# Kernel tuning notes

Measured on AMD Instinct MI355X. Metric: run time of the kernel, lower is better.

Reference implementation:

```python
import jax, jax.numpy as jnp
import numpy as np

D_RBF = 36
KMIN = 9
EPS_LN = 1e-5


def layer_norm(x, g, b):
    mu = x.mean(-1, keepdims=True)
    var = ((x - mu) ** 2).mean(-1, keepdims=True)
    return (x - mu) * jax.lax.rsqrt(var + EPS_LN) * g + b


def rbf(D):
    # radial basis expansion, 36 gaussians on [0, 20]
    mu = jnp.linspace(0.0, 20.0, D_RBF)
    sigma = 20.0 / D_RBF
    return jnp.exp(-(((D[..., None] - mu) / sigma) ** 2))


def cdist(a, b):
    d2 = jnp.sum((a[:, :, None, :] - b[:, None, :, :]) ** 2, -1)
    return jnp.sqrt(jnp.maximum(d2, 1e-12))


def setup_inputs() -> dict:
    key = jax.random.key(0)
    ks = iter(jax.random.split(key, 64))
    B, N, L = 1, 64, 512
    d_msa, d_pair, d_state = 64, 128, 16
    def nrm(shape, s=1.0):
        return jax.random.normal(next(ks), shape, jnp.float32) * s
    def lin(fin, fout):
        return nrm((fin, fout), 0.05), jnp.zeros((fout,), jnp.float32)
    def ln(d):
        return jnp.ones((d,), jnp.float32), jnp.zeros((d,), jnp.float32)
    inp = {}
    inp['msa'] = nrm((B, N, L, d_msa))
    inp['pair'] = nrm((B, L, L, d_pair))
    inp['xyz'] = nrm((B, L, 3, 3), 8.0)  # spread coords so kNN is meaningful
    inp['state'] = nrm((B, L, d_state))
    inp['seq1hot'] = jax.nn.one_hot(jax.random.randint(next(ks), (B, L), 0, 21), 21, dtype=jnp.float32)
    inp['idx'] = jnp.broadcast_to(jnp.arange(L, dtype=jnp.int32)[None], (B, L))
    inp['top_k'] = 64
    inp['g_msa'], inp['b_msa'] = ln(d_msa)
    inp['g_pair'], inp['b_pair'] = ln(d_pair)
    inp['g_state'], inp['b_state'] = ln(d_state)
    inp['Wq'], inp['bq'] = lin(d_msa, d_msa)
    inp['Wk'], inp['bk'] = lin(d_msa, d_msa)
    inp['Wx'], inp['bx'] = lin(d_msa + 21 + d_state, 32)
    inp['We1'], inp['be1'] = lin(d_pair, 32)
    inp['We2'], inp['be2'] = lin(32 + D_RBF + 1, 32)
    inp['g_node'], inp['b_node'] = ln(32)
    inp['g_e1'], inp['b_e1'] = ln(32)
    inp['g_e2'], inp['b_e2'] = ln(32)
    # SE3-style equivariant MP layer params
    inp['Wm1'], inp['bm1'] = lin(32 + 32 + 32 + 1, 64)
    inp['Wm2'], inp['bm2'] = lin(64, 32)
    inp['Wc'], inp['bc'] = lin(32, 8)      # 2 out vec channels x (1 coef for d + 3 for v_src)
    inp['Wh'], inp['bh'] = lin(64, 16)     # l0 out
    inp['Wv'] = nrm((2, 3), 0.05)          # l1 channel mixing
    return inp


def reference(msa, pair, xyz, state, seq1hot, idx, top_k,
              g_msa, b_msa, g_pair, b_pair, g_state, b_state,
              Wq, bq, Wk, bk, Wx, bx, We1, be1, We2, be2,
              g_node, b_node, g_e1, b_e1, g_e2, b_e2,
              Wm1, bm1, Wm2, bm2, Wc, bc, Wh, bh, Wv):
    eps = 1e-5
    B, N, L, K = msa.shape
    msa = layer_norm(msa, g_msa, b_msa)
    pair = layer_norm(pair, g_pair, b_pair)
    state = layer_norm(state, g_state, b_state)

    # SequenceWeight (1 head): first-seq query attends over N sequences per position
    q = (msa[:, 0] @ Wq + bq) / jnp.sqrt(jnp.float32(K))       # (B,L,K)
    k = jnp.einsum('bnlk,kd->bnld', msa, Wk) + bk              # (B,N,L,K)
    attn = jax.nn.softmax(jnp.einsum('blk,bnlk->bnl', q, k), axis=1)
    msa1 = jnp.einsum('bnl,bnlk->blk', attn, msa)              # (B,L,K)

    node = jnp.concatenate([msa1, seq1hot, state], -1)
    node = layer_norm(node @ Wx + bx, g_node, b_node)          # (B,L,32)
    edge = layer_norm(pair @ We1 + be1, g_e1, b_e1)            # (B,L,L,32)

    sep = idx[:, None, :] - idx[:, :, None]                    # (B,L,L)
    neighbor = jnp.where(jnp.abs(sep) <= 1, sep, 0).astype(node.dtype)[..., None]
    ca = xyz[:, :, 1]                                          # (B,L,3)
    rbf_feat = rbf(cdist(ca, ca))
    edge = jnp.concatenate([edge, rbf_feat, neighbor], -1)
    edge = layer_norm(edge @ We2 + be2, g_e2, b_e2)            # (B,L,L,32)

    # kNN + sequence-separation graph, as a dense boolean mask (edge i->j)
    eye = jnp.eye(L)[None]
    D = cdist(ca, ca) + eye * 999.9
    sep_a = jnp.abs(sep).astype(jnp.float32) + eye * 999.9
    kk = min(int(top_k), L)
    _, E_idx = jax.lax.top_k(-jax.lax.stop_gradient(D), kk)    # (B,L,kk) nearest j per i
    bi = jnp.arange(B)[:, None, None]
    ii = jnp.arange(L)[None, :, None]
    mask = jnp.zeros((B, L, L), bool).at[bi, ii, E_idx].set(True)
    mask = jnp.logical_or(mask, sep_a < KMIN)
    maskf = mask.astype(node.dtype)

    v = xyz - ca[:, :, None, :]                                # l1 feats (B,L,3,3)
    dvec = jax.lax.stop_gradient(ca[:, None, :, :] - ca[:, :, None, :])  # d[b,i,j]=ca_j-ca_i
    dist = jnp.linalg.norm(dvec, axis=-1, keepdims=True)       # (B,L,L,1)

    # invariant scalar messages (avoid materializing concat: split Wm1)
    hid = (node @ Wm1[:32])[:, :, None, :] + (node @ Wm1[32:64])[:, None, :, :] \
        + edge @ Wm1[64:96] + dist * Wm1[96] + bm1
    hid = jax.nn.relu(hid)                                     # (B,L,L,64)
    m = jax.nn.relu(hid @ Wm2 + bm2)                           # (B,L,L,32)
    coef = (m @ Wc + bc).reshape(B, L, L, 2, 4)
    # equivariant vector messages: coef0 * d_ij + sum_c coef_c * v_i[c]
    vmsg = coef[..., 0:1] * dvec[:, :, :, None, :] \
         + jnp.einsum('bijoc,bicv->bijov', coef[..., 1:], v)   # (B,L,L,2,3)
    agg_m = jnp.einsum('bij,bijk->bjk', maskf, m)              # aggregate at target j
    agg_v = jnp.einsum('bij,bijov->bjov', maskf, vmsg)

    state_out = jnp.concatenate([node, agg_m], -1) @ Wh + bh   # shift['0'] -> (B,L,16)
    off = agg_v + jnp.einsum('oc,blcv->blov', Wv, v)           # shift['1'] -> (B,L,2,3)

    # Rodrigues rotation + translation update
    T = off[:, :, 0]
    R = off[:, :, 1]
    ang = jnp.linalg.norm(R, axis=-1, keepdims=True)           # (B,L,1)
    Rv = (R / (ang + eps))[:, :, None, :]                      # (B,L,1,3)
    Rdv = jnp.sum(Rv * v, -1, keepdims=True)                   # (B,L,3,1)
    Rxv = jnp.cross(jnp.broadcast_to(Rv, v.shape), v)
    vperp = v - Rv * Rdv
    upar = Rv * Rdv
    c = jnp.cos(ang)[:, :, None, :]
    s = jnp.sin(ang)[:, :, None, :]
    v_new = vperp * c + Rxv * s + upar
    xyz_new = v_new + (ca + T)[:, :, None, :]
    return xyz_new, state_out
```

## Files before the change

### kernel.cpp

```cpp
#include <hip/hip_runtime.h>
#include <hip/hip_bf16.h>

typedef __attribute__((ext_vector_type(8))) short short8v;
typedef __attribute__((ext_vector_type(4))) float f32x4;

__device__ __forceinline__ unsigned short f2bu(float a){
  union { __hip_bfloat16 b; unsigned short u; } cv;
  cv.b = __float2bfloat16(a);
  return cv.u;
}
__device__ __forceinline__ void sp2(float a, unsigned short &h, unsigned short &l){
  h = f2bu(a);
  l = f2bu(a - __uint_as_float(((unsigned)h)<<16));
}
__device__ __forceinline__ float wred64(float v){
  #pragma unroll
  for(int o=32;o;o>>=1) v += __shfl_xor(v,o,64);
  return v;
}
__device__ __forceinline__ float wred32(float v){
  #pragma unroll
  for(int o=16;o;o>>=1) v += __shfl_xor(v,o,64);
  return v;
}
__device__ __forceinline__ float wmax64(float v){
  #pragma unroll
  for(int o=32;o;o>>=1) v = fmaxf(v,__shfl_xor(v,o,64));
  return v;
}

__global__ void __launch_bounds__(256) k_ctx(
  const float* __restrict__ msa, const float* __restrict__ g_msa, const float* __restrict__ b_msa,
  const float* __restrict__ Wq, const float* __restrict__ bq,
  const float* __restrict__ Wk, const float* __restrict__ bk,
  const float* __restrict__ seq1hot, const float* __restrict__ state,
  const float* __restrict__ g_state, const float* __restrict__ b_state,
  const float* __restrict__ Wx, const float* __restrict__ bx,
  const float* __restrict__ g_node, const float* __restrict__ b_node,
  const float* __restrict__ Wm1, const float* __restrict__ xyz,
  float* __restrict__ node, float* __restrict__ nodeA, float* __restrict__ nodeB,
  float* __restrict__ ca, float* __restrict__ vv)
{
  int l = blockIdx.x, tid = threadIdx.x;
  int wave = tid>>6, lane = tid&63;
  __shared__ float ms[64][64];
  __shared__ float qs[64];
  __shared__ float logit[64];
  __shared__ float part[4][64];
  __shared__ float ins[101];
  __shared__ float nd[32];

  {
    int nn = tid>>2, qd = tid&3;
    const float* mrow = msa + ((size_t)nn*512 + (size_t)l)*64 + qd*16;
    f32x4 a[4];
    #pragma unroll
    for(int t=0;t<4;t++) a[t] = *(const f32x4*)(mrow + t*4);
    float s=0.f, ss=0.f;
    #pragma unroll
    for(int t=0;t<4;t++)
      #pragma unroll
      for(int e=0;e<4;e++){ float v=a[t][e]; s+=v; ss+=v*v; }
    s  += __shfl_xor(s,1,64);  s  += __shfl_xor(s,2,64);
    ss += __shfl_xor(ss,1,64); ss += __shfl_xor(ss,2,64);
    float mu = s*(1.f/64.f);
    float rstd = rsqrtf(ss*(1.f/64.f) - mu*mu + 1e-5f);
    #pragma unroll
    for(int t=0;t<4;t++){
      f32x4 g4 = *(const f32x4*)(g_msa + qd*16 + t*4);
      f32x4 b4 = *(const f32x4*)(b_msa + qd*16 + t*4);
      f32x4 o4;
      #pragma unroll
      for(int e=0;e<4;e++) o4[e] = (a[t][e]-mu)*rstd*g4[e] + b4[e];
      *(f32x4*)&ms[nn][qd*16 + t*4] = o4;
    }
  }
  __syncthreads();
  if(wave==0){
    float acc = bq[lane];
    for(int k=0;k<64;k++) acc += ms[0][k]*Wq[k*64+lane];
    qs[lane] = acc*0.125f;
  }
  __syncthreads();
  float qd2 = qs[lane];
  for(int it=0; it<16; ++it){
    int nn = it*4 + wave;
    float acc = bk[lane];
    for(int k2=0;k2<64;k2++) acc += ms[nn][k2]*Wk[k2*64+lane];
    float p = wred64(qd2*acc);
    if(lane==0) logit[nn] = p;
  }
  __syncthreads();
  float v  = logit[lane];
  float mx = wmax64(v);
  float e  = expf(v-mx);
  float sd = wred64(e);
  float a  = e/sd;
  float pm = 0.f;
  for(int it=0; it<16; ++it){
    int nn = it*4 + wave;
    pm += __shfl(a,nn,64)*ms[nn][lane];
  }
  part[wave][lane] = pm;
  __syncthreads();
  if(wave==0){
    ins[lane] = part[0][lane]+part[1][lane]+part[2][lane]+part[3][lane];
    if(lane<21) ins[64+lane] = seq1hot[l*21+lane];
    float sv = (lane<16)? state[l*16+lane] : 0.f;
    float mu = sv;
    #pragma unroll
    for(int o=8;o;o>>=1) mu += __shfl_xor(mu,o,64);
    mu *= (1.f/16.f);
    float dv = sv-mu;
    float var = dv*dv;
    #pragma unroll
    for(int o=8;o;o>>=1) var += __shfl_xor(var,o,64);
    var *= (1.f/16.f);
    if(lane<16) ins[85+lane] = dv*rsqrtf(var+1e-5f)*g_state[lane]+b_state[lane];

    int d = lane & 31;
    float np_ = 0.f;
    if(lane<32){
      np_ = bx[d];
      for(int c=0;c<101;c++) np_ += ins[c]*Wx[c*32+d];
    }
    float mu2 = wred32(np_)*(1.f/32.f);
    float d2  = np_-mu2;
    float v2  = wred32(d2*d2)*(1.f/32.f);
    float nv  = d2*rsqrtf(v2+1e-5f);
    if(lane<32){
      nv = nv*g_node[d]+b_node[d];
      node[l*32+d] = nv;
      nd[d] = nv;
    }
    float a2=0.f, b2=0.f;
    for(int c=0;c<32;c++){
      float x = nd[c];
      a2 += x*Wm1[c*64+lane];
      b2 += x*Wm1[(32+c)*64+lane];
    }
    nodeA[l*64+lane] = a2;
    nodeB[l*64+lane] = b2;
    if(lane<3) ca[l*3+lane] = xyz[l*9+3+lane];
    if(lane<9) vv[l*9+lane] = xyz[l*9+lane] - xyz[l*9+3+(lane%3)];
  }
}

__global__ void k_topk(const float* __restrict__ ca, const int* __restrict__ idx,
                       const int* __restrict__ topk_ptr, unsigned char* __restrict__ maskT){
  int i = blockIdx.x, lane = threadIdx.x;
  float cx = ca[i*3], cy = ca[i*3+1], cz = ca[i*3+2];
  int idxi = idx[i];
  unsigned long long key[8];
  #pragma unroll
  for(int t=0;t<8;t++){
    int jj = t*64 + lane;
    float dx = cx-ca[jj*3], dy = cy-ca[jj*3+1], dz = cz-ca[jj*3+2];
    float dd = sqrtf(fmaxf(dx*dx+dy*dy+dz*dz, 1e-12f));
    if(jj==i) dd += 999.9f;
    key[t] = (((unsigned long long)__float_as_uint(dd))<<32) | (unsigned)jj;
    int sep = abs(idx[jj]-idxi);
    maskT[jj*512+i] = (jj!=i && sep<9) ? 1 : 0;
  }
  int kk = *topk_ptr; if(kk>512) kk = 512;
  for(int t=0;t<kk;t++){
    unsigned long long m = key[0];
    #pragma unroll
    for(int u=1;u<8;u++) m = (key[u]<m)? key[u] : m;
    #pragma unroll
    for(int o=32;o;o>>=1){
      unsigned long long o2 = __shfl_xor(m,o,64);
      m = (o2<m)? o2 : m;
    }
    int jc = (int)(m & 0xffffffffu);
    if(lane==0) maskT[jc*512+i] = 1;
    #pragma unroll
    for(int u=0;u<8;u++) if(key[u]==m) key[u] = ~0ull;
  }
}

__global__ void k_fold(const float* __restrict__ We1, const float* __restrict__ be1,
                       const float* __restrict__ g_pair, const float* __restrict__ b_pair,
                       const float* __restrict__ We2, const float* __restrict__ be2,
                       const float* __restrict__ g_e1, const float* __restrict__ b_e1,
                       const float* __restrict__ Wm1, const float* __restrict__ bm1,
                       const float* __restrict__ g_e2, const float* __restrict__ b_e2,
                       const float* __restrict__ Wm2, const float* __restrict__ Wc,
                       unsigned short* __restrict__ wbuf, float* __restrict__ bbuf){
  int fidx = blockIdx.x;
  int tid  = threadIdx.x;
  if(fidx < 46){
    int t = fidx*512 + tid;
    int lane = tid>>3, e = tid&7;
    int f = (fidx<23)? fidx : fidx-23;
    int krow = (lane>>4)*8 + e;
    int n = lane&15;
    float val = 0.f;
    if(f<8){
      int kt=f>>1, nt=f&1; int c=kt*32+krow, d=nt*16+n;
      val = g_pair[c]*We1[c*32+d];
    } else if(f<14){
      int f2=f-8; int kt=f2>>1, nt=f2&1; int c=kt*32+krow, d=nt*16+n;
      if(c<32)      val = g_e1[c]*We2[c*32+d];
      else if(c<69) val = We2[c*32+d];
      else          val = 0.f;
    } else if(f<18){
      int nt=f-14; int c=krow, h=nt*16+n;
      val = g_e2[c]*Wm1[(64+c)*64+h];
    } else if(f<22){
      int f2=f-18; int kt=f2>>1, nt=f2&1; int c=kt*32+krow, d=nt*16+n;
      val = Wm2[c*32+d];
    } else {
      int c=krow;
      val = (n<8)? Wc[c*8+n] : 0.f;
    }
    unsigned short h = f2bu(val);
    if(fidx<23) wbuf[t] = h;
    else {
      float fh = __uint_as_float(((unsigned)h)<<16);
      wbuf[t] = f2bu(val - fh);
    }
  } else {
    if(tid<32){
      float s = be1[tid];
      for(int c=0;c<128;c++) s += b_pair[c]*We1[c*32+tid];
      bbuf[tid]=s;
    } else if(tid<64){
      int d=tid-32; float s=be2[d];
      for(int c=0;c<32;c++) s += b_e1[c]*We2[c*32+d];
      bbuf[tid]=s;
    } else if(tid<128){
      int h=tid-64; float s=bm1[h];
      for(int c=0;c<32;c++) s += b_e2[c]*Wm1[(64+c)*64+h];
      bbuf[tid]=s;
    }
  }
}

__global__ void __launch_bounds__(256,2) k_pair_mfma(
  const float* __restrict__ pair, const unsigned short* __restrict__ wbuf,
  const float* __restrict__ bbuf, const float* __restrict__ Wm1,
  const float* __restrict__ bm2, const float* __restrict__ bc,
  const float* __restrict__ nodeA, const float* __restrict__ nodeB,
  const float* __restrict__ ca, const float* __restrict__ vv,
  const int* __restrict__ idx, const unsigned char* __restrict__ maskT,
  float* __restrict__ aggM, float* __restrict__ aggV)
{
  const int j = blockIdx.x, tid = threadIdx.x;
  const int wave = tid>>6, lane = tid&63;
  const int kg = lane>>4, n = lane&15;

  __shared__ __align__(16) unsigned short Yh[4][16*104];
  __shared__ __align__(16) unsigned short Yl[4][16*104];
  __shared__ __align__(16) unsigned short WloE[23*512];
  __shared__ float coefT[4][16*8];
  __shared__ float redM[4][32];
  __shared__ float redV[4][8];
  unsigned short* Yhw = Yh[wave];
  unsigned short* Ylw = Yl[wave];
  float* CT = coefT[wave];

  for(int t=tid; t<(23*512)/8; t+=256)
    ((uint4*)WloE)[t] = ((const uint4*)(wbuf + 23*512))[t];

  short8v wf[23];
  #pragma unroll
  for(int f=0; f<23; f++) wf[f] = *(const short8v*)(wbuf + f*512 + lane*8);

  const float be1f0 = bbuf[n],     be1f1 = bbuf[16+n];
  const float be2f0 = bbuf[32+n],  be2f1 = bbuf[48+n];
  float bm1f[4], wm1d[4], nodeBj[4];
  #pragma unroll
  for(int nt=0;nt<4;nt++){
    bm1f[nt]   = bbuf[64+nt*16+n];
    wm1d[nt]   = Wm1[96*64+nt*16+n];
    nodeBj[nt] = nodeB[j*64+nt*16+n];
  }
  const float bm2r0 = bm2[n], bm2r1 = bm2[16+n];
  const float bcr = (n<8)? bc[n] : 0.f;
  const float cjx = ca[j*3], cjy = ca[j*3+1], cjz = ca[j*3+2];
  const int idxj = idx[j];

  __syncthreads();

  for(int t=lane; t<16*27; t+=64){ int r=t/27, c=69+t-r*27; Yhw[r*104+c]=0; Ylw[r*104+c]=0; }

  float accM0=0.f, accM1=0.f;
  float accV[6]={0.f,0.f,0.f,0.f,0.f,0.f};

  float x[4][8];
  {
    const float* prow0 = pair + (((size_t)(wave*16+n))*512 + (size_t)j)*128;
    #pragma unroll
    for(int kt=0;kt<4;kt++){
      *(f32x4*)&x[kt][0] = *(const f32x4*)(prow0 + kt*32 + kg*8);
      *(f32x4*)&x[kt][4] = *(const f32x4*)(prow0 + kt*32 + kg*8 + 4);
    }
  }

  for(int i0 = wave*16; i0 < 512; i0 += 64){
    float s=0.f, ss=0.f;
    #pragma unroll
    for(int kt=0;kt<4;kt++)
      #pragma unroll
      for(int e=0;e<8;e++){ float xv=x[kt][e]; s+=xv; ss+=xv*xv; }
    s  += __shfl_xor(s,16,64);  s  += __shfl_xor(s,32,64);
    ss += __shfl_xor(ss,16,64); ss += __shfl_xor(ss,32,64);
    float mu = s*(1.f/128.f);
    float rstd = rsqrtf(ss*(1.f/128.f) - mu*mu + 1e-5f);
    short8v xh[4], xl[4];
    #pragma unroll
    for(int kt=0;kt<4;kt++){
      #pragma unroll
      for(int e=0;e<8;e++){
        unsigned short h_, l_;
        sp2((x[kt][e]-mu)*rstd, h_, l_);
        xh[kt][e] = (short)h_;
        xl[kt][e] = (short)l_;
      }
    }

    float xn[4][8];
    const bool hasNext = (i0+64 < 512);
    if(hasNext){
      const float* prown = pair + (((size_t)(i0+64+n))*512 + (size_t)j)*128;
      #pragma unroll
      for(int kt=0;kt<4;kt++){
        *(f32x4*)&xn[kt][0] = *(const f32x4*)(prown + kt*32 + kg*8);
        *(f32x4*)&xn[kt][4] = *(const f32x4*)(prown + kt*32 + kg*8 + 4);
      }
    }

    f32x4 z0={0.f,0.f,0.f,0.f}, z1={0.f,0.f,0.f,0.f};
    #pragma unroll
    for(int kt=0;kt<4;kt++){
      short8v wlo0 = *(const short8v*)&WloE[(2*kt+0)*512 + lane*8];
      short8v wlo1 = *(const short8v*)&WloE[(2*kt+1)*512 + lane*8];
      z0 = __builtin_amdgcn_mfma_f32_16x16x32_bf16(xh[kt], wf[2*kt+0], z0, 0,0,0);
      z0 = __builtin_amdgcn_mfma_f32_16x16x32_bf16(xl[kt], wf[2*kt+0], z0, 0,0,0);
      z0 = __builtin_amdgcn_mfma_f32_16x16x32_bf16(xh[kt], wlo0,      z0, 0,0,0);
      z1 = __builtin_amdgcn_mfma_f32_16x16x32_bf16(xh[kt], wf[2*kt+1], z1, 0,0,0);
      z1 = __builtin_amdgcn_mfma_f32_16x16x32_bf16(xl[kt], wf[2*kt+1], z1, 0,0,0);
      z1 = __builtin_amdgcn_mfma_f32_16x16x32_bf16(xh[kt], wlo1,      z1, 0,0,0);
    }
    #pragma unroll
    for(int q=0;q<4;q++){
      float ev0 = z0[q] + be1f0;
      float ev1 = z1[q] + be1f1;
      float sq  = ev0+ev1;
      float sq2 = ev0*ev0+ev1*ev1;
      #pragma unroll
      for(int o=8;o;o>>=1){ sq+=__shfl_xor(sq,o,64); sq2+=__shfl_xor(sq2,o,64); }
      float m_ = sq*(1.f/32.f);
      float rs = rsqrtf(sq2*(1.f/32.f)-m_*m_+1e-5f);
      unsigned short h0,l0,h1,l1;
      sp2((ev0-m_)*rs, h0, l0);
      sp2((ev1-m_)*rs, h1, l1);
      int r = 4*kg+q;
      Yhw[r*104 + n]    = h0;
      Yhw[r*104 + 16+n] = h1;
      Ylw[r*104 + n]    = l0;
      Ylw[r*104 + 16+n] = l1;
    }

    const float* cai = ca + (i0+n)*3;
    float dxr = cjx-cai[0], dyr = cjy-cai[1], dzr = cjz-cai[2];
    float d2r = dxr*dxr+dyr*dyr+dzr*dzr;
    float dist_r = sqrtf(d2r);
    float drbf = sqrtf(fmaxf(d2r,1e-12f));
    #pragma unroll
    for(int sI=0;sI<9;sI++){
      int t = kg*9+sI;
      float u = (drbf - (float)t*(20.f/35.f))*1.8f;
      unsigned short h_, l_;
      sp2(__expf(-u*u), h_, l_);
      Yhw[n*104 + 32 + t] = h_;
      Ylw[n*104 + 32 + t] = l_;
    }
    if(kg==0){
      int sep = idxj - idx[i0+n];
      float nb = (sep>=-1 && sep<=1)?(float)sep:0.f;
      unsigned short h_, l_;
      sp2(nb, h_, l_);
      Yhw[n*104 + 68] = h_;
      Ylw[n*104 + 68] = l_;
    }

    short8v yh_[3], yl_[3];
    #pragma unroll
    for(int kt=0;kt<3;kt++){
      yh_[kt] = *(const short8v*)&Yhw[n*104 + kt*32 + kg*8];
      yl_[kt] = *(const short8v*)&Ylw[n*104 + kt*32 + kg*8];
    }
    f32x4 e2a0={0.f,0.f,0.f,0.f}, e2a1={0.f,0.f,0.f,0.f};
    #pragma unroll
    for(int kt=0;kt<3;kt++){
      short8v wlo0 = *(const short8v*)&WloE[(8+2*kt)*512 + lane*8];
      short8v wlo1 = *(const short8v*)&WloE[(9+2*kt)*512 + lane*8];
      e2a0 = __builtin_amdgcn_mfma_f32_16x16x32_bf16(yh_[kt], wf[8+2*kt], e2a0, 0,0,0);
      e2a0 = __builtin_amdgcn_mfma_f32_16x16x32_bf16(yl_[kt], wf[8+2*kt], e2a0, 0,0,0);
      e2a0 = __builtin_amdgcn_mfma_f32_16x16x32_bf16(yh_[kt], wlo0,      e2a0, 0,0,0);
      e2a1 = __builtin_amdgcn_mfma_f32_16x16x32_bf16(yh_[kt], wf[9+2*kt], e2a1, 0,0,0);
      e2a1 = __builtin_amdgcn_mfma_f32_16x16x32_bf16(yl_[kt], wf[9+2*kt], e2a1, 0,0,0);
      e2a1 = __builtin_amdgcn_mfma_f32_16x16x32_bf16(yh_[kt], wlo1,      e2a1, 0,0,0);
    }
    #pragma unroll
    for(int q=0;q<4;q++){
      float ev0 = e2a0[q]+be2f0;
      float ev1 = e2a1[q]+be2f1;
      float sq  = ev0+ev1;
      float sq2 = ev0*ev0+ev1*ev1;
      #pragma unroll
      for(int o=8;o;o>>=1){ sq+=__shfl_xor(sq,o,64); sq2+=__shfl_xor(sq2,o,64); }
      float m_ = sq*(1.f/32.f);
      float rs = rsqrtf(sq2*(1.f/32.f)-m_*m_+1e-5f);
      unsigned short h0,l0,h1,l1;
      sp2((ev0-m_)*rs, h0, l0);
      sp2((ev1-m_)*rs, h1, l1);
      int r = 4*kg+q;
      Yhw[r*104 + n]    = h0;
      Yhw[r*104 + 16+n] = h1;
      Ylw[r*104 + n]    = l0;
      Ylw[r*104 + 16+n] = l1;
    }

    short8v e2Ah = *(const short8v*)&Yhw[n*104 + kg*8];
    short8v e2Al = *(const short8v*)&Ylw[n*104 + kg*8];
    float dist_q[4];
    #pragma unroll
    for(int q=0;q<4;q++) dist_q[q] = __shfl(dist_r, 4*kg+q, 64);
    #pragma unroll
    for(int nt=0;nt<4;nt++){
      short8v wlo = *(const short8v*)&WloE[(14+nt)*512 + lane*8];
      f32x4 hacc = {0.f,0.f,0.f,0.f};
      hacc = __builtin_amdgcn_mfma_f32_16x16x32_bf16(e2Ah, wf[14+nt], hacc, 0,0,0);
      hacc = __builtin_amdgcn_mfma_f32_16x16x32_bf16(e2Al, wf[14+nt], hacc, 0,0,0);
      hacc = __builtin_amdgcn_mfma_f32_16x16x32_bf16(e2Ah, wlo,       hacc, 0,0,0);
      #pragma unroll
      for(int q=0;q<4;q++){
        float t_ = hacc[q] + bm1f[nt] + nodeBj[nt] + dist_q[q]*wm1d[nt]
                 + nodeA[(i0+4*kg+q)*64 + nt*16+n];
        float hv = fmaxf(t_,0.f);
        unsigned short h_, l_;
        sp2(hv, h_, l_);
        Yhw[(4*kg+q)*104 + nt*16+n] = h_;
        Ylw[(4*kg+q)*104 + nt*16+n] = l_;
      }
    }

    short8v hAh[2], hAl[2];
    #pragma unroll
    for(int kt=0;kt<2;kt++){
      hAh[kt] = *(const short8v*)&Yhw[n*104 + kt*32 + kg*8];
      hAl[kt] = *(const short8v*)&Ylw[n*104 + kt*32 + kg*8];
    }
    f32x4 ma0={0.f,0.f,0.f,0.f}, ma1={0.f,0.f,0.f,0.f};
    #pragma unroll
    for(int kt=0;kt<2;kt++){
      short8v wlo0 = *(const short8v*)&WloE[(18+2*kt)*512 + lane*8];
      short8v wlo1 = *(const short8v*)&WloE[(19+2*kt)*512 + lane*8];
      ma0 = __builtin_amdgcn_mfma_f32_16x16x32_bf16(hAh[kt], wf[18+2*kt], ma0, 0,0,0);
      ma0 = __builtin_amdgcn_mfma_f32_16x16x32_bf16(hAl[kt], wf[18+2*kt], ma0, 0,0,0);
      ma0 = __builtin_amdgcn_mfma_f32_16x16x32_bf16(hAh[kt], wlo0,       ma0, 0,0,0);
      ma1 = __builtin_amdgcn_mfma_f32_16x16x32_bf16(hAh[kt], wf[19+2*kt], ma1, 0,0,0);
      ma1 = __builtin_amdgcn_mfma_f32_16x16x32_bf16(hAl[kt], wf[19+2*kt], ma1, 0,0,0);
      ma1 = __builtin_amdgcn_mfma_f32_16x16x32_bf16(hAh[kt], wlo1,       ma1, 0,0,0);
    }
    float mk[4];
    #pragma unroll
    for(int q=0;q<4;q++) mk[q] = (float)maskT[j*512 + i0+4*kg+q];
    #pragma unroll
    for(int q=0;q<4;q++){
      float mv0 = fmaxf(ma0[q]+bm2r0, 0.f);
      float mv1 = fmaxf(ma1[q]+bm2r1, 0.f);
      accM0 += mk[q]*mv0;
      accM1 += mk[q]*mv1;
      unsigned short h0,l0,h1,l1;
      sp2(mv0, h0, l0);
      sp2(mv1, h1, l1);
      int r = 4*kg+q;
      Yhw[r*104 + n]    = h0;
      Yhw[r*104 + 16+n] = h1;
      Ylw[r*104 + n]    = l0;
      Ylw[r*104 + 16+n] = l1;
    }

    short8v mAh = *(const short8v*)&Yhw[n*104 + kg*8];
    short8v mAl = *(const short8v*)&Ylw[n*104 + kg*8];
    short8v wloC = *(const short8v*)&WloE[22*512 + lane*8];
    f32x4 cf = {0.f,0.f,0.f,0.f};
    cf = __builtin_amdgcn_mfma_f32_16x16x32_bf16(mAh, wf[22], cf, 0,0,0);
    cf = __builtin_amdgcn_mfma_f32_16x16x32_bf16(mAl, wf[22], cf, 0,0,0);
    cf = __builtin_amdgcn_mfma_f32_16x16x32_bf16(mAh, wloC,  cf, 0,0,0);
    if(n<8){
      #pragma unroll
      for(int q=0;q<4;q++) CT[(4*kg+q)*8+n] = cf[q]+bcr;
    }
    f32x4 cA = *(const f32x4*)&CT[n*8];
    f32x4 cB = *(const f32x4*)&CT[n*8+4];

    float mkr = (float)maskT[j*512 + i0+n];
    const float* vr = vv + (i0+n)*9;
    float v00=vr[0], v01=vr[1], v02=vr[2];
    float v10=vr[3], v11=vr[4], v12=vr[5];
    float v20=vr[6], v21=vr[7], v22=vr[8];
    accV[0] += mkr*(cA[0]*dxr + cA[1]*v00 + cA[2]*v10 + cA[3]*v20);
    accV[1] += mkr*(cA[0]*dyr + cA[1]*v01 + cA[2]*v11 + cA[3]*v21);
    accV[2] += mkr*(cA[0]*dzr + cA[1]*v02 + cA[2]*v12 + cA[3]*v22);
    accV[3] += mkr*(cB[0]*dxr + cB[1]*v00 + cB[2]*v10 + cB[3]*v20);
    accV[4] += mkr*(cB[0]*dyr + cB[1]*v01 + cB[2]*v11 + cB[3]*v21);
    accV[5] += mkr*(cB[0]*dzr + cB[1]*v02 + cB[2]*v12 + cB[3]*v22);

    if(hasNext){
      #pragma unroll
      for(int kt=0;kt<4;kt++)
        #pragma unroll
        for(int e=0;e<8;e++) x[kt][e] = xn[kt][e];
    }
  }

  accM0 += __shfl_xor(accM0,16,64); accM0 += __shfl_xor(accM0,32,64);
  accM1 += __shfl_xor(accM1,16,64); accM1 += __shfl_xor(accM1,32,64);
  #pragma unroll
  for(int c=0;c<6;c++){
    #pragma unroll
    for(int o=8;o;o>>=1) accV[c] += __shfl_xor(accV[c],o,64);
  }
  if(lane<16){ redM[wave][n] = accM0; redM[wave][16+n] = accM1; }
  if(lane==0){
    #pragma unroll
    for(int c=0;c<6;c++) redV[wave][c]=accV[c];
  }
  __syncthreads();
  if(tid<32) aggM[j*32+tid] = redM[0][tid]+redM[1][tid]+redM[2][tid]+redM[3][tid];
  if(tid>=64 && tid<70){
    int c = tid-64;
    aggV[j*6+c] = redV[0][c]+redV[1][c]+redV[2][c]+redV[3][c];
  }
}

__global__ void k_final(const float* __restrict__ node, const float* __restrict__ aggM,
                        const float* __restrict__ aggV, const float* __restrict__ Wh,
                        const float* __restrict__ bh, const float* __restrict__ Wv,
                        const float* __restrict__ ca, const float* __restrict__ vvb,
                        float* __restrict__ out){
  int l = blockIdx.x, lane = threadIdx.x;
  if(lane<16){
    float acc = bh[lane];
    for(int c=0;c<32;c++) acc += node[l*32+c]*Wh[c*16+lane];
    for(int c=0;c<32;c++) acc += aggM[l*32+c]*Wh[(32+c)*16+lane];
    out[4608 + l*16 + lane] = acc;
  }
  if(lane<9){
    int a = lane/3, vd = lane%3;
    float T[3], R[3];
    for(int q2=0;q2<3;q2++){
      float v0 = vvb[l*9+q2], v1 = vvb[l*9+3+q2], v2 = vvb[l*9+6+q2];
      T[q2] = aggV[l*6+q2]   + Wv[0]*v0 + Wv[1]*v1 + Wv[2]*v2;
      R[q2] = aggV[l*6+3+q2] + Wv[3]*v0 + Wv[4]*v1 + Wv[5]*v2;
    }
    float ang = sqrtf(R[0]*R[0]+R[1]*R[1]+R[2]*R[2]);
    float inv = 1.f/(ang+1e-5f);
    float Rv0=R[0]*inv, Rv1=R[1]*inv, Rv2=R[2]*inv;
    float va0=vvb[l*9+a*3+0], va1=vvb[l*9+a*3+1], va2=vvb[l*9+a*3+2];
    float Rdv = Rv0*va0+Rv1*va1+Rv2*va2;
    float Rvv[3]={Rv0,Rv1,Rv2};
    float vaa[3]={va0,va1,va2};
    float Rxv = Rvv[(vd+1)%3]*vaa[(vd+2)%3] - Rvv[(vd+2)%3]*vaa[(vd+1)%3];
    float vperp = vaa[vd] - Rvv[vd]*Rdv;
    float upar  = Rvv[vd]*Rdv;
    float cc = cosf(ang), ss = sinf(ang);
    float vnew = vperp*cc + Rxv*ss + upar;
    out[l*9+a*3+vd] = vnew + ca[l*3+vd] + T[vd];
  }
}

extern "C" void kernel_launch(void* const* d_in, const int* in_sizes, int n_in,
                              void* d_out, int out_size, void* d_ws, size_t ws_size,
                              hipStream_t stream) {
  const float* msa    = (const float*)d_in[0];
  const float* pair   = (const float*)d_in[1];
  const float* xyz    = (const float*)d_in[2];
  const float* state  = (const float*)d_in[3];
  const float* seq1hot= (const float*)d_in[4];
  const int*   idx    = (const int*)d_in[5];
  const int*   topk   = (const int*)d_in[6];
  const float* g_msa  = (const float*)d_in[7];  const float* b_msa  = (const float*)d_in[8];
  const float* g_pair = (const float*)d_in[9];  const float* b_pair = (const float*)d_in[10];
  const float* g_state= (const float*)d_in[11]; const float* b_state= (const float*)d_in[12];
  const float* Wq = (const float*)d_in[13]; const float* bq = (const float*)d_in[14];
  const float* Wk = (const float*)d_in[15]; const float* bk = (const float*)d_in[16];
  const float* Wx = (const float*)d_in[17]; const float* bx = (const float*)d_in[18];
  const float* We1= (const float*)d_in[19]; const float* be1= (const float*)d_in[20];
  const float* We2= (const float*)d_in[21]; const float* be2= (const float*)d_in[22];
  const float* g_node=(const float*)d_in[23]; const float* b_node=(const float*)d_in[24];
  const float* g_e1 = (const float*)d_in[25]; const float* b_e1 = (const float*)d_in[26];
  const float* g_e2 = (const float*)d_in[27]; const float* b_e2 = (const float*)d_in[28];
  const float* Wm1= (const float*)d_in[29]; const float* bm1= (const float*)d_in[30];
  const float* Wm2= (const float*)d_in[31]; const float* bm2= (const float*)d_in[32];
  const float* Wc = (const float*)d_in[33]; const float* bc = (const float*)d_in[34];
  const float* Wh = (const float*)d_in[35]; const float* bh = (const float*)d_in[36];
  const float* Wv = (const float*)d_in[37];
  float* out = (float*)d_out;

  float* ws = (float*)d_ws;
  float* node   = ws; ws += 512*32;
  float* nodeA  = ws; ws += 512*64;
  float* nodeB  = ws; ws += 512*64;
  float* cab    = ws; ws += 512*3;
  float* vvb    = ws; ws += 512*9;
  float* aggM   = ws; ws += 512*32;
  float* aggV   = ws; ws += 512*6;
  float* bbuf   = ws; ws += 160;
  unsigned short* wbuf = (unsigned short*)ws; ws += (46*512)/2 + 8;
  unsigned char* maskT = (unsigned char*)ws;

  k_fold<<<47,512,0,stream>>>(We1,be1,g_pair,b_pair,We2,be2,g_e1,b_e1,Wm1,bm1,g_e2,b_e2,Wm2,Wc,wbuf,bbuf);
  k_ctx<<<512,256,0,stream>>>(msa,g_msa,b_msa,Wq,bq,Wk,bk,seq1hot,state,g_state,b_state,
                              Wx,bx,g_node,b_node,Wm1,xyz,node,nodeA,nodeB,cab,vvb);
  k_topk<<<512,64,0,stream>>>(cab,idx,topk,maskT);
  k_pair_mfma<<<512,256,0,stream>>>(pair,wbuf,bbuf,Wm1,bm2,bc,nodeA,nodeB,cab,vvb,idx,maskT,aggM,aggV);
  k_final<<<512,64,0,stream>>>(node,aggM,aggV,Wh,bh,Wv,cab,vvb,out);
}
```

Baseline: 123.3 us.

## Merge top-k into context kernel and hoist per-tile loads in pair kernel

The ca/vv coordinate prep moves into an extra block of the weight-folding kernel. The kNN top-k selection runs on wave 1 of the context kernel instead of a separate launch, which removes one kernel launch and its dependency gap. In the pair MFMA kernel, the next-tile prefetch, nodeA, mask, vv, ca and idx loads are issued before the bf16 split so their latency overlaps compute, and the two biases are pre-summed. Holding these values longer raises register pressure, and the top-k wave adds serial work inside the context kernel's blocks.

```diff
diff --git a/kernel.cpp b/kernel.cpp
--- a/kernel.cpp
+++ b/kernel.cpp
@@ -37,9 +37,10 @@
   const float* __restrict__ g_state, const float* __restrict__ b_state,
   const float* __restrict__ Wx, const float* __restrict__ bx,
   const float* __restrict__ g_node, const float* __restrict__ b_node,
-  const float* __restrict__ Wm1, const float* __restrict__ xyz,
+  const float* __restrict__ Wm1,
   float* __restrict__ node, float* __restrict__ nodeA, float* __restrict__ nodeB,
-  float* __restrict__ ca, float* __restrict__ vv)
+  const float* __restrict__ ca, const int* __restrict__ idx,
+  const int* __restrict__ topk_ptr, unsigned char* __restrict__ maskT)
 {
   int l = blockIdx.x, tid = threadIdx.x;
   int wave = tid>>6, lane = tid&63;
@@ -141,41 +142,36 @@
     }
     nodeA[l*64+lane] = a2;
     nodeB[l*64+lane] = b2;
-    if(lane<3) ca[l*3+lane] = xyz[l*9+3+lane];
-    if(lane<9) vv[l*9+lane] = xyz[l*9+lane] - xyz[l*9+3+(lane%3)];
-  }
-}
-
-__global__ void k_topk(const float* __restrict__ ca, const int* __restrict__ idx,
-                       const int* __restrict__ topk_ptr, unsigned char* __restrict__ maskT){
-  int i = blockIdx.x, lane = threadIdx.x;
-  float cx = ca[i*3], cy = ca[i*3+1], cz = ca[i*3+2];
-  int idxi = idx[i];
-  unsigned long long key[8];
-  #pragma unroll
-  for(int t=0;t<8;t++){
-    int jj = t*64 + lane;
-    float dx = cx-ca[jj*3], dy = cy-ca[jj*3+1], dz = cz-ca[jj*3+2];
-    float dd = sqrtf(fmaxf(dx*dx+dy*dy+dz*dz, 1e-12f));
-    if(jj==i) dd += 999.9f;
-    key[t] = (((unsigned long long)__float_as_uint(dd))<<32) | (unsigned)jj;
-    int sep = abs(idx[jj]-idxi);
-    maskT[jj*512+i] = (jj!=i && sep<9) ? 1 : 0;
-  }
-  int kk = *topk_ptr; if(kk>512) kk = 512;
-  for(int t=0;t<kk;t++){
-    unsigned long long m = key[0];
-    #pragma unroll
-    for(int u=1;u<8;u++) m = (key[u]<m)? key[u] : m;
-    #pragma unroll
-    for(int o=32;o;o>>=1){
-      unsigned long long o2 = __shfl_xor(m,o,64);
-      m = (o2<m)? o2 : m;
-    }
-    int jc = (int)(m & 0xffffffffu);
-    if(lane==0) maskT[jc*512+i] = 1;
-    #pragma unroll
-    for(int u=0;u<8;u++) if(key[u]==m) key[u] = ~0ull;
+  } else if(wave==1){
+    int i = l;
+    float cx = ca[i*3], cy = ca[i*3+1], cz = ca[i*3+2];
+    int idxi = idx[i];
+    unsigned long long key[8];
+    #pragma unroll
+    for(int t=0;t<8;t++){
+      int jj = t*64 + lane;
+      float dx = cx-ca[jj*3], dy = cy-ca[jj*3+1], dz = cz-ca[jj*3+2];
+      float dd = sqrtf(fmaxf(dx*dx+dy*dy+dz*dz, 1e-12f));
+      if(jj==i) dd += 999.9f;
+      key[t] = (((unsigned long long)__float_as_uint(dd))<<32) | (unsigned)jj;
+      int sep = abs(idx[jj]-idxi);
+      maskT[jj*512+i] = (jj!=i && sep<9) ? 1 : 0;
+    }
+    int kk = *topk_ptr; if(kk>512) kk = 512;
+    for(int t=0;t<kk;t++){
+      unsigned long long m = key[0];
+      #pragma unroll
+      for(int u=1;u<8;u++) m = (key[u]<m)? key[u] : m;
+      #pragma unroll
+      for(int o=32;o;o>>=1){
+        unsigned long long o2 = __shfl_xor(m,o,64);
+        m = (o2<m)? o2 : m;
+      }
+      int jc = (int)(m & 0xffffffffu);
+      if(lane==0) maskT[jc*512+i] = 1;
+      #pragma unroll
+      for(int u=0;u<8;u++) if(key[u]==m) key[u] = ~0ull;
+    }
   }
 }
 
@@ -186,7 +182,9 @@
                        const float* __restrict__ Wm1, const float* __restrict__ bm1,
                        const float* __restrict__ g_e2, const float* __restrict__ b_e2,
                        const float* __restrict__ Wm2, const float* __restrict__ Wc,
-                       unsigned short* __restrict__ wbuf, float* __restrict__ bbuf){
+                       const float* __restrict__ xyz,
+                       unsigned short* __restrict__ wbuf, float* __restrict__ bbuf,
+                       float* __restrict__ ca, float* __restrict__ vv){
   int fidx = blockIdx.x;
   int tid  = threadIdx.x;
   if(fidx < 46){
@@ -220,7 +218,7 @@
       float fh = __uint_as_float(((unsigned)h)<<16);
       wbuf[t] = f2bu(val - fh);
     }
-  } else {
+  } else if(fidx == 46){
     if(tid<32){
       float s = be1[tid];
       for(int c=0;c<128;c++) s += b_pair[c]*We1[c*32+tid];
@@ -234,6 +232,16 @@
       for(int c=0;c<32;c++) s += b_e2[c]*Wm1[(64+c)*64+h];
       bbuf[tid]=s;
     }
+  } else {
+    int l = tid;
+    float c0=xyz[l*9+3], c1=xyz[l*9+4], c2=xyz[l*9+5];
+    ca[l*3+0]=c0; ca[l*3+1]=c1; ca[l*3+2]=c2;
+    #pragma unroll
+    for(int a2=0;a2<3;a2++){
+      vv[l*9+a2*3+0]=xyz[l*9+a2*3+0]-c0;
+      vv[l*9+a2*3+1]=xyz[l*9+a2*3+1]-c1;
+      vv[l*9+a2*3+2]=xyz[l*9+a2*3+2]-c2;
+    }
   }
 }
 
@@ -269,12 +277,11 @@
 
   const float be1f0 = bbuf[n],     be1f1 = bbuf[16+n];
   const float be2f0 = bbuf[32+n],  be2f1 = bbuf[48+n];
-  float bm1f[4], wm1d[4], nodeBj[4];
+  float bm1n[4], wm1d[4];
   #pragma unroll
   for(int nt=0;nt<4;nt++){
-    bm1f[nt]   = bbuf[64+nt*16+n];
-    wm1d[nt]   = Wm1[96*64+nt*16+n];
-    nodeBj[nt] = nodeB[j*64+nt*16+n];
+    bm1n[nt] = bbuf[64+nt*16+n] + nodeB[j*64+nt*16+n];
+    wm1d[nt] = Wm1[96*64+nt*16+n];
   }
   const float bm2r0 = bm2[n], bm2r1 = bm2[16+n];
   const float bcr = (n<8)? bc[n] : 0.f;
@@ -308,6 +315,36 @@
     ss += __shfl_xor(ss,16,64); ss += __shfl_xor(ss,32,64);
     float mu = s*(1.f/128.f);
     float rstd = rsqrtf(ss*(1.f/128.f) - mu*mu + 1e-5f);
+
+    float xn[4][8];
+    const bool hasNext = (i0+64 < 512);
+    if(hasNext){
+      const float* prown = pair + (((size_t)(i0+64+n))*512 + (size_t)j)*128;
+      #pragma unroll
+      for(int kt=0;kt<4;kt++){
+        *(f32x4*)&xn[kt][0] = *(const f32x4*)(prown + kt*32 + kg*8);
+        *(f32x4*)&xn[kt][4] = *(const f32x4*)(prown + kt*32 + kg*8 + 4);
+      }
+    }
+
+    float na[4][4];
+    #pragma unroll
+    for(int q=0;q<4;q++)
+      #pragma unroll
+      for(int nt=0;nt<4;nt++)
+        na[nt][q] = nodeA[(size_t)(i0+4*kg+q)*64 + nt*16+n];
+    float mk[4];
+    #pragma unroll
+    for(int q=0;q<4;q++) mk[q] = (float)maskT[j*512 + i0+4*kg+q];
+    float mkr = (float)maskT[j*512 + i0+n];
+    const float* vr = vv + (i0+n)*9;
+    float v00=vr[0], v01=vr[1], v02=vr[2];
+    float v10=vr[3], v11=vr[4], v12=vr[5];
+    float v20=vr[6], v21=vr[7], v22=vr[8];
+    const float* cai = ca + (i0+n)*3;
+    float cix=cai[0], ciy=cai[1], ciz=cai[2];
+    int idxi_r = idx[i0+n];
+
     short8v xh[4], xl[4];
     #pragma unroll
     for(int kt=0;kt<4;kt++){
@@ -317,17 +354,6 @@
         sp2((x[kt][e]-mu)*rstd, h_, l_);
         xh[kt][e] = (short)h_;
         xl[kt][e] = (short)l_;
-      }
-    }
-
-    float xn[4][8];
-    const bool hasNext = (i0+64 < 512);
-    if(hasNext){
-      const float* prown = pair + (((size_t)(i0+64+n))*512 + (size_t)j)*128;
-      #pragma unroll
-      for(int kt=0;kt<4;kt++){
-        *(f32x4*)&xn[kt][0] = *(const f32x4*)(prown + kt*32 + kg*8);
-        *(f32x4*)&xn[kt][4] = *(const f32x4*)(prown + kt*32 + kg*8 + 4);
       }
     }
 
@@ -363,8 +389,7 @@
       Ylw[r*104 + 16+n] = l1;
     }
 
-    const float* cai = ca + (i0+n)*3;
-    float dxr = cjx-cai[0], dyr = cjy-cai[1], dzr = cjz-cai[2];
+    float dxr = cjx-cix, dyr = cjy-ciy, dzr = cjz-ciz;
     float d2r = dxr*dxr+dyr*dyr+dzr*dzr;
     float dist_r = sqrtf(d2r);
     float drbf = sqrtf(fmaxf(d2r,1e-12f));
@@ -378,7 +403,7 @@
       Ylw[n*104 + 32 + t] = l_;
     }
     if(kg==0){
-      int sep = idxj - idx[i0+n];
+      int sep = idxj - idxi_r;
       float nb = (sep>=-1 && sep<=1)?(float)sep:0.f;
       unsigned short h_, l_;
       sp2(nb, h_, l_);
@@ -438,8 +463,7 @@
       hacc = __builtin_amdgcn_mfma_f32_16x16x32_bf16(e2Ah, wlo,       hacc, 0,0,0);
       #pragma unroll
       for(int q=0;q<4;q++){
-        float t_ = hacc[q] + bm1f[nt] + nodeBj[nt] + dist_q[q]*wm1d[nt]
-                 + nodeA[(i0+4*kg+q)*64 + nt*16+n];
+        float t_ = hacc[q] + bm1n[nt] + dist_q[q]*wm1d[nt] + na[nt][q];
         float hv = fmaxf(t_,0.f);
         unsigned short h_, l_;
         sp2(hv, h_, l_);
@@ -466,9 +490,6 @@
       ma1 = __builtin_amdgcn_mfma_f32_16x16x32_bf16(hAl[kt], wf[19+2*kt], ma1, 0,0,0);
       ma1 = __builtin_amdgcn_mfma_f32_16x16x32_bf16(hAh[kt], wlo1,       ma1, 0,0,0);
     }
-    float mk[4];
-    #pragma unroll
-    for(int q=0;q<4;q++) mk[q] = (float)maskT[j*512 + i0+4*kg+q];
     #pragma unroll
     for(int q=0;q<4;q++){
       float mv0 = fmaxf(ma0[q]+bm2r0, 0.f);
@@ -499,11 +520,6 @@
     f32x4 cA = *(const f32x4*)&CT[n*8];
     f32x4 cB = *(const f32x4*)&CT[n*8+4];
 
-    float mkr = (float)maskT[j*512 + i0+n];
-    const float* vr = vv + (i0+n)*9;
-    float v00=vr[0], v01=vr[1], v02=vr[2];
-    float v10=vr[3], v11=vr[4], v12=vr[5];
-    float v20=vr[6], v21=vr[7], v22=vr[8];
     accV[0] += mkr*(cA[0]*dxr + cA[1]*v00 + cA[2]*v10 + cA[3]*v20);
     accV[1] += mkr*(cA[0]*dyr + cA[1]*v01 + cA[2]*v11 + cA[3]*v21);
     accV[2] += mkr*(cA[0]*dzr + cA[1]*v02 + cA[2]*v12 + cA[3]*v22);
@@ -615,10 +631,10 @@
   unsigned short* wbuf = (unsigned short*)ws; ws += (46*512)/2 + 8;
   unsigned char* maskT = (unsigned char*)ws;
 
-  k_fold<<<47,512,0,stream>>>(We1,be1,g_pair,b_pair,We2,be2,g_e1,b_e1,Wm1,bm1,g_e2,b_e2,Wm2,Wc,wbuf,bbuf);
+  k_fold<<<48,512,0,stream>>>(We1,be1,g_pair,b_pair,We2,be2,g_e1,b_e1,Wm1,bm1,g_e2,b_e2,Wm2,Wc,
+                              xyz,wbuf,bbuf,cab,vvb);
   k_ctx<<<512,256,0,stream>>>(msa,g_msa,b_msa,Wq,bq,Wk,bk,seq1hot,state,g_state,b_state,
-                              Wx,bx,g_node,b_node,Wm1,xyz,node,nodeA,nodeB,cab,vvb);
-  k_topk<<<512,64,0,stream>>>(cab,idx,topk,maskT);
+                              Wx,bx,g_node,b_node,Wm1,node,nodeA,nodeB,cab,idx,topk,maskT);
   k_pair_mfma<<<512,256,0,stream>>>(pair,wbuf,bbuf,Wm1,bm2,bc,nodeA,nodeB,cab,vvb,idx,maskT,aggM,aggV);
   k_final<<<512,64,0,stream>>>(node,aggM,aggV,Wh,bh,Wv,cab,vvb,out);
 }
```

Result: faster. 113.2 us (-8.2%).
